# Performance work log

Hardware: AMD Instinct MI355X
Metric: run time of the kernel (lower is better)

The kernel has to match this reference:

```python
import jax, jax.numpy as jnp
import numpy as np

B, T, D_IN, D_PROJ, D_OUT, MEM = 8, 2048, 1024, 1024, 1024, 40


def setup_inputs() -> dict:
    key = jax.random.key(0)
    k1, k2, k3, k4 = jax.random.split(key, 4)
    x = jax.random.normal(k1, (B, T, D_IN), dtype=jnp.float32)
    # xavier-uniform-style params
    lim1 = np.sqrt(6.0 / (D_IN + D_PROJ))
    lim2 = np.sqrt(6.0 / (D_PROJ + D_OUT))
    limm = np.sqrt(6.0 / (MEM + 1 + D_PROJ))
    W1 = jax.random.uniform(k2, (D_IN, D_PROJ), minval=-lim1, maxval=lim1, dtype=jnp.float32)
    W2 = jax.random.uniform(k3, (D_PROJ, D_OUT), minval=-lim2, maxval=lim2, dtype=jnp.float32)
    mw = jax.random.uniform(k4, (MEM + 1, D_PROJ), minval=-limm, maxval=limm, dtype=jnp.float32)
    mw = mw.at[0].set(0.0)  # row 0 zeroed at init (still trainable in the original)
    bias1 = jnp.ones((D_PROJ,), dtype=jnp.float32)
    bias2 = jnp.ones((D_OUT,), dtype=jnp.float32)
    return {"input_data": x, "W1": W1, "bias1": bias1, "W2": W2, "bias2": bias2,
            "memory_weights": mw}


def _fsmn_memory(p, memory_weights):
    # p: [B, T, D], memory_weights: [M+1, D]
    # Original gather index: mm[i,j] = i-j+1 for 0<=i-j<=M-1, else 0.
    # => out[b,i,d] = sum_{l=0}^{M-1} w[l+1,d]*p[b,i-l,d]
    #              + w[0,d] * (sum_j p[b,j,d] - sum_{l=0}^{M-1} p[b,i-l,d])
    M = memory_weights.shape[0] - 1
    b, t, d = p.shape
    # causal depthwise conv: taps w[1:] with lag l -> kernel position M-1-l
    rhs = memory_weights[1:][::-1].T[:, None, :]           # [D, 1, M]
    lhs = jnp.pad(p.transpose(0, 2, 1), ((0, 0), (0, 0), (M - 1, 0)))  # [B, D, T+M-1]
    band = jax.lax.conv_general_dilated(
        lhs, rhs, window_strides=(1,), padding='VALID',
        feature_group_count=d,
        dimension_numbers=('NCH', 'OIH', 'NCH')).transpose(0, 2, 1)    # [B, T, D]
    # in-band running sum via cumsum difference
    cs = jnp.cumsum(p, axis=1)                              # [B, T, D]
    band_sum = cs - jnp.pad(cs, ((0, 0), (M, 0), (0, 0)))[:, :t]
    total = cs[:, -1:]                                      # [B, 1, D]
    return band + memory_weights[0] * (total - band_sum)


def reference(input_data, W1, bias1, W2, bias2, memory_weights):
    p = jnp.matmul(input_data, W1) + bias1                  # [B, T, D_PROJ]
    p = _fsmn_memory(p, memory_weights)
    return jnp.matmul(p, W2) + bias2                        # [B, T, D_OUT]
```

## Files before the change

kernel.cpp:

```cpp
#include <hip/hip_runtime.h>

typedef __attribute__((ext_vector_type(8))) short bf16x8;
typedef __attribute__((ext_vector_type(4))) float f32x4;
typedef __attribute__((ext_vector_type(8))) unsigned short u16x8;

typedef const __attribute__((address_space(1))) void* as1cv;
typedef __attribute__((address_space(3))) void* as3v;

__device__ __forceinline__ unsigned short f2bf(float f) {
    union { float f; unsigned u; } x; x.f = f;
    unsigned r = x.u + 0x7FFFu + ((x.u >> 16) & 1u);
    return (unsigned short)(r >> 16);
}
__device__ __forceinline__ float bf2f(unsigned short u) {
    union { unsigned u; float f; } x; x.u = ((unsigned)u) << 16; return x.f;
}

__global__ void k_cvt_bf16(const float* __restrict__ in, unsigned short* __restrict__ out, long n) {
    long i = (long)blockIdx.x * blockDim.x + threadIdx.x;
    long stride = (long)gridDim.x * blockDim.x;
    long n4 = n >> 2;
    for (long j = i; j < n4; j += stride) {
        float4 v = ((const float4*)in)[j];
        ushort4 o;
        o.x = f2bf(v.x); o.y = f2bf(v.y); o.z = f2bf(v.z); o.w = f2bf(v.w);
        ((ushort4*)out)[j] = o;
    }
}

__global__ void k_transpose_bf16(const float* __restrict__ W, unsigned short* __restrict__ Wt,
                                 int rows, int cols) {
    __shared__ float tile[64][65];
    int r0 = blockIdx.y * 64, c0 = blockIdx.x * 64;
    #pragma unroll
    for (int i = 0; i < 16; ++i) {
        int idx = threadIdx.x + i * 256;
        int r = idx >> 6, c = idx & 63;
        tile[r][c] = W[(long)(r0 + r) * cols + (c0 + c)];
    }
    __syncthreads();
    #pragma unroll
    for (int i = 0; i < 16; ++i) {
        int idx = threadIdx.x + i * 256;
        int r = idx >> 6, c = idx & 63;
        Wt[(long)(c0 + r) * rows + (r0 + c)] = f2bf(tile[c][r]);
    }
}

template<int OUT_BF16>
__global__ __launch_bounds__(512, 2) void k_gemm256(
    const unsigned short* __restrict__ A,
    const unsigned short* __restrict__ Bt,
    const float* __restrict__ bias,
    void* __restrict__ C,
    int M, int N, int K)
{
    __shared__ unsigned short lds[2][4][8192];
    const int tid  = threadIdx.x;
    const int lane = tid & 63;
    const int w    = tid >> 6;
    const int wm   = w >> 2;
    const int wn   = w & 3;

    const int nwg = gridDim.x;
    const int cpx = nwg >> 3;
    const int wg  = (blockIdx.x & 7) * cpx + (blockIdx.x >> 3);
    const int nblks = N >> 8;
    const int mblk = wg / nblks, nblk = wg % nblks;
    const long m0 = (long)mblk << 8, n0 = (long)nblk << 8;

    const int segRow  = lane >> 3;
    const long segColE = (long)(((lane & 7) ^ segRow) << 3);

    const int rr = lane & 15, cc = lane >> 4;
    const int smask = (rr & 7) << 4;
    const int colSwz0 = (((cc * 16) ^ smask) >> 1);
    const int colSwz1 = (((64 + cc * 16) ^ smask) >> 1);

    auto stage = [&](int buf, int slot, const unsigned short* src, long rowBase, int kt) {
        #pragma unroll
        for (int g = 0; g < 2; ++g) {
            const int s = w + g * 8;
            const unsigned short* gp = src + (rowBase + s * 8 + segRow) * (long)K
                                           + (long)kt * 64 + segColE;
            __builtin_amdgcn_global_load_lds((as1cv)gp,
                (as3v)(&lds[buf][slot][s * 512 + lane * 8]), 16, 0, 0);
        }
    };

    f32x4 acc[8][4];
    #pragma unroll
    for (int i = 0; i < 8; ++i)
        #pragma unroll
        for (int j = 0; j < 4; ++j)
            acc[i][j] = (f32x4){0.f, 0.f, 0.f, 0.f};

    bf16x8 bfrag[4][2];
    const int bRowBase = (wn & 1) * 64;
    const int NK = K >> 6;
    const int ITERS = K >> 7;

#define VM4   asm volatile("s_waitcnt vmcnt(4)" ::: "memory")
#define PHASE(BUF, Q, STAGES, VMW) do {                                              \
    bf16x8 af0_0, af0_1, af1_0, af1_1;                                               \
    { const unsigned short* Ah = &lds[BUF][wm][0];                                   \
      af0_0 = *(const bf16x8*)(Ah + ((Q)*32 + rr) * 64 + colSwz0);                   \
      af0_1 = *(const bf16x8*)(Ah + ((Q)*32 + rr) * 64 + colSwz1);                   \
      af1_0 = *(const bf16x8*)(Ah + ((Q)*32 + 16 + rr) * 64 + colSwz0);              \
      af1_1 = *(const bf16x8*)(Ah + ((Q)*32 + 16 + rr) * 64 + colSwz1); }            \
    if ((Q) == 0) { const unsigned short* Bh = &lds[BUF][2 + (wn >> 1)][0];          \
      _Pragma("unroll")                                                              \
      for (int nj = 0; nj < 4; ++nj) {                                               \
        bfrag[nj][0] = *(const bf16x8*)(Bh + (bRowBase + nj*16 + rr) * 64 + colSwz0);\
        bfrag[nj][1] = *(const bf16x8*)(Bh + (bRowBase + nj*16 + rr) * 64 + colSwz1);\
      } }                                                                            \
    STAGES;                                                                          \
    VMW;                                                                             \
    __builtin_amdgcn_s_barrier();                                                    \
    asm volatile("s_waitcnt lgkmcnt(0)" ::: "memory");                               \
    __builtin_amdgcn_sched_barrier(0);                                               \
    __builtin_amdgcn_s_setprio(1);                                                   \
    _Pragma("unroll")                                                                \
    for (int nj = 0; nj < 4; ++nj) {                                                 \
      acc[2*(Q)][nj]   = __builtin_amdgcn_mfma_f32_16x16x32_bf16(af0_0, bfrag[nj][0], acc[2*(Q)][nj],   0,0,0); \
      acc[2*(Q)][nj]   = __builtin_amdgcn_mfma_f32_16x16x32_bf16(af0_1, bfrag[nj][1], acc[2*(Q)][nj],   0,0,0); \
      acc[2*(Q)+1][nj] = __builtin_amdgcn_mfma_f32_16x16x32_bf16(af1_0, bfrag[nj][0], acc[2*(Q)+1][nj], 0,0,0); \
      acc[2*(Q)+1][nj] = __builtin_amdgcn_mfma_f32_16x16x32_bf16(af1_1, bfrag[nj][1], acc[2*(Q)+1][nj], 0,0,0); \
    }                                                                                \
    __builtin_amdgcn_s_setprio(0);                                                   \
    __builtin_amdgcn_s_barrier();                                                    \
} while (0)

    stage(0, 0, A,  m0,       0);
    stage(0, 1, A,  m0 + 128, 0);
    stage(0, 2, Bt, n0,       0);
    stage(0, 3, Bt, n0 + 128, 0);
    stage(1, 2, Bt, n0,       1);
    stage(1, 3, Bt, n0 + 128, 1);
    VM4;
    __builtin_amdgcn_s_barrier();

    for (int it = 0; it < ITERS; ++it) {
        const int kt1 = 2 * it + 1;
        int kt2 = 2 * it + 2; if (kt2 >= NK) kt2 = 0;
        int kt3 = 2 * it + 3; if (kt3 >= NK) kt3 = 1;

        PHASE(0, 0, stage(1, 0, A,  m0,       kt1), );
        PHASE(0, 1, stage(1, 1, A,  m0 + 128, kt1), );
        PHASE(0, 2, { stage(0, 2, Bt, n0, kt2); stage(0, 3, Bt, n0 + 128, kt2); }, );
        PHASE(0, 3, , VM4);
        PHASE(1, 0, stage(0, 0, A,  m0,       kt2), );
        PHASE(1, 1, stage(0, 1, A,  m0 + 128, kt2), );
        PHASE(1, 2, { stage(1, 2, Bt, n0, kt3); stage(1, 3, Bt, n0 + 128, kt3); }, );
        PHASE(1, 3, , VM4);
    }
#undef PHASE
#undef VM4

    #pragma unroll
    for (int mi = 0; mi < 8; ++mi) {
        const long rowb = m0 + wm * 128 + mi * 16 + cc * 4;
        #pragma unroll
        for (int nj = 0; nj < 4; ++nj) {
            const long col = n0 + wn * 64 + nj * 16 + rr;
            const float bv = bias[col];
            #pragma unroll
            for (int jj = 0; jj < 4; ++jj) {
                const float v = acc[mi][nj][jj] + bv;
                if (OUT_BF16) ((unsigned short*)C)[(rowb + jj) * N + col] = f2bf(v);
                else          ((float*)C)[(rowb + jj) * N + col] = v;
            }
        }
    }
}

__global__ void k_colsum(const unsigned short* __restrict__ p, float* __restrict__ total, int T) {
    const int b = blockIdx.y;
    const int t0 = blockIdx.x * 64;
    const int tid = threadIdx.x;
    float s0 = 0.f, s1 = 0.f, s2 = 0.f, s3 = 0.f;
    const unsigned short* base = p + ((long)b * T + t0) * 1024 + tid * 4;
    for (int t = 0; t < 64; ++t) {
        ushort4 v = *(const ushort4*)(base + (long)t * 1024);
        s0 += bf2f(v.x); s1 += bf2f(v.y); s2 += bf2f(v.z); s3 += bf2f(v.w);
    }
    float* tp = total + b * 1024 + tid * 4;
    atomicAdd(tp + 0, s0); atomicAdd(tp + 1, s1);
    atomicAdd(tp + 2, s2); atomicAdd(tp + 3, s3);
}

#define FS_ROWS 167
__global__ __launch_bounds__(256, 2) void k_fsmn(
    const unsigned short* __restrict__ p,
    const float* __restrict__ mw,
    const float* __restrict__ total,
    unsigned short* __restrict__ p2,
    int T)
{
    __shared__ unsigned short sp[FS_ROWS][64];
    __shared__ float smw[41][64];
    const int b  = blockIdx.z;
    const int t0 = blockIdx.y * 128;
    const int d0 = blockIdx.x * 64;
    const int tid = threadIdx.x;

    for (int idx = tid; idx < 41 * 64; idx += 256) {
        int r = idx >> 6, c = idx & 63;
        smw[r][c] = mw[r * 1024 + d0 + c];
    }
    {
        const int row0 = tid >> 3;
        const int col8 = (tid & 7) * 8;
        #pragma unroll
        for (int i = 0; i < 6; ++i) {
            const int row = row0 + i * 32;
            if (row < FS_ROWS) {
                const int t = t0 + row - 39;
                u16x8 v = {0, 0, 0, 0, 0, 0, 0, 0};
                if (t >= 0)
                    v = *(const u16x8*)(p + ((long)b * T + t) * 1024 + d0 + col8);
                *(u16x8*)(&sp[row][col8]) = v;
            }
        }
    }
    __syncthreads();

    const int lane = tid & 63, wv = tid >> 6;
    const int d = d0 + lane;

    float m[40];
    #pragma unroll
    for (int l = 0; l < 40; ++l) m[l] = smw[l + 1][lane];
    const float m0v = smw[0][lane];
    const float tot = total[b * 1024 + d];

    #pragma unroll
    for (int pass = 0; pass < 2; ++pass) {
        const int obase = wv * 32 + pass * 16;
        float w[55];
        #pragma unroll
        for (int j = 0; j < 55; ++j) w[j] = bf2f(sp[obase + j][lane]);

        float acc[16];
        #pragma unroll
        for (int s = 0; s < 16; ++s) acc[s] = 0.f;
        #pragma unroll
        for (int lag = 0; lag < 40; ++lag) {
            const float mm = m[lag];
            #pragma unroll
            for (int s = 0; s < 16; ++s)
                acc[s] = fmaf(mm, w[s + 39 - lag], acc[s]);
        }

        float accw[16];
        {
            float S = 0.f;
            #pragma unroll
            for (int j = 0; j < 40; ++j) S += w[j];
            accw[0] = S;
            #pragma unroll
            for (int s = 1; s < 16; ++s) accw[s] = accw[s - 1] + w[s + 39] - w[s - 1];
        }

        unsigned short* ob = p2 + ((long)b * T + t0 + obase) * 1024 + d;
        #pragma unroll
        for (int s = 0; s < 16; ++s)
            ob[(long)s * 1024] = f2bf(acc[s] + m0v * (tot - accw[s]));
    }
}

extern "C" void kernel_launch(void* const* d_in, const int* in_sizes, int n_in,
                              void* d_out, int out_size, void* d_ws, size_t ws_size,
                              hipStream_t stream) {
    const float* x  = (const float*)d_in[0];
    const float* W1 = (const float*)d_in[1];
    const float* b1 = (const float*)d_in[2];
    const float* W2 = (const float*)d_in[3];
    const float* b2 = (const float*)d_in[4];
    const float* mw = (const float*)d_in[5];
    float* out = (float*)d_out;

    const int B = 8, T = 2048;
    const long M = (long)B * T;
    const int N = 1024, K = 1024;

    char* ws = (char*)d_ws;
    unsigned short* x_bf   = (unsigned short*)(ws);
    unsigned short* W1t    = (unsigned short*)(ws + 33554432L);
    unsigned short* W2t    = (unsigned short*)(ws + 35651584L);
    unsigned short* p_bf   = (unsigned short*)(ws + 37748736L);
    float*          totals = (float*)(ws + 71303168L);
    unsigned short* p2_bf  = x_bf;

    k_cvt_bf16<<<2048, 256, 0, stream>>>(x, x_bf, M * 1024);

    dim3 tgrid(16, 16);
    k_transpose_bf16<<<tgrid, 256, 0, stream>>>(W1, W1t, K, N);
    k_transpose_bf16<<<tgrid, 256, 0, stream>>>(W2, W2t, K, N);

    k_gemm256<1><<<dim3((int)((M / 256) * (N / 256))), 512, 0, stream>>>(
        x_bf, W1t, b1, (void*)p_bf, (int)M, N, K);

    hipMemsetAsync(totals, 0, B * 1024 * sizeof(float), stream);
    k_colsum<<<dim3(T / 64, B), 256, 0, stream>>>(p_bf, totals, T);

    k_fsmn<<<dim3(1024 / 64, T / 128, B), 256, 0, stream>>>(p_bf, mw, totals, p2_bf, T);

    k_gemm256<0><<<dim3((int)((M / 256) * (N / 256))), 512, 0, stream>>>(
        p2_bf, W2t, b2, (void*)out, (int)M, N, K);
}
```

Measured before the change: 137.7 us.

## Fuse column-sum into first GEMM epilogue and vectorize stores via swapped MFMA operands

Swaps the MFMA operand order so each lane holds four consecutive output columns. The epilogue can then write packed bf16x4 or float4 stores instead of scalar ones. The first GEMM also reduces per-column sums across lanes and atomically adds them into the per-batch totals, so the separate colsum kernel and its re-read of p are removed. The two weight transposes are merged into one launch. Costs are more atomics from many blocks and a slightly heavier epilogue; the fused sums are taken in fp32 before bf16 rounding, which shifts numerics slightly.

```diff
diff --git a/kernel.cpp b/kernel.cpp
--- a/kernel.cpp
+++ b/kernel.cpp
@@ -28,8 +28,11 @@
     }
 }
 
-__global__ void k_transpose_bf16(const float* __restrict__ W, unsigned short* __restrict__ Wt,
-                                 int rows, int cols) {
+__global__ void k_transpose_bf16(const float* __restrict__ W1, unsigned short* __restrict__ W1t,
+                                 const float* __restrict__ W2, unsigned short* __restrict__ W2t) {
+    const int rows = 1024, cols = 1024;
+    const float* W = blockIdx.z ? W2 : W1;
+    unsigned short* Wt = blockIdx.z ? W2t : W1t;
     __shared__ float tile[64][65];
     int r0 = blockIdx.y * 64, c0 = blockIdx.x * 64;
     #pragma unroll
@@ -47,12 +50,13 @@
     }
 }
 
-template<int OUT_BF16>
+template<int OUT_BF16, int DO_COLSUM>
 __global__ __launch_bounds__(512, 2) void k_gemm256(
     const unsigned short* __restrict__ A,
     const unsigned short* __restrict__ Bt,
     const float* __restrict__ bias,
     void* __restrict__ C,
+    float* __restrict__ totals,
     int M, int N, int K)
 {
     __shared__ unsigned short lds[2][4][8192];
@@ -88,11 +92,11 @@
         }
     };
 
-    f32x4 acc[8][4];
-    #pragma unroll
-    for (int i = 0; i < 8; ++i)
-        #pragma unroll
-        for (int j = 0; j < 4; ++j)
+    f32x4 acc[4][8];
+    #pragma unroll
+    for (int i = 0; i < 4; ++i)
+        #pragma unroll
+        for (int j = 0; j < 8; ++j)
             acc[i][j] = (f32x4){0.f, 0.f, 0.f, 0.f};
 
     bf16x8 bfrag[4][2];
@@ -122,10 +126,10 @@
     __builtin_amdgcn_s_setprio(1);                                                   \
     _Pragma("unroll")                                                                \
     for (int nj = 0; nj < 4; ++nj) {                                                 \
-      acc[2*(Q)][nj]   = __builtin_amdgcn_mfma_f32_16x16x32_bf16(af0_0, bfrag[nj][0], acc[2*(Q)][nj],   0,0,0); \
-      acc[2*(Q)][nj]   = __builtin_amdgcn_mfma_f32_16x16x32_bf16(af0_1, bfrag[nj][1], acc[2*(Q)][nj],   0,0,0); \
-      acc[2*(Q)+1][nj] = __builtin_amdgcn_mfma_f32_16x16x32_bf16(af1_0, bfrag[nj][0], acc[2*(Q)+1][nj], 0,0,0); \
-      acc[2*(Q)+1][nj] = __builtin_amdgcn_mfma_f32_16x16x32_bf16(af1_1, bfrag[nj][1], acc[2*(Q)+1][nj], 0,0,0); \
+      acc[nj][2*(Q)]   = __builtin_amdgcn_mfma_f32_16x16x32_bf16(bfrag[nj][0], af0_0, acc[nj][2*(Q)],   0,0,0); \
+      acc[nj][2*(Q)]   = __builtin_amdgcn_mfma_f32_16x16x32_bf16(bfrag[nj][1], af0_1, acc[nj][2*(Q)],   0,0,0); \
+      acc[nj][2*(Q)+1] = __builtin_amdgcn_mfma_f32_16x16x32_bf16(bfrag[nj][0], af1_0, acc[nj][2*(Q)+1], 0,0,0); \
+      acc[nj][2*(Q)+1] = __builtin_amdgcn_mfma_f32_16x16x32_bf16(bfrag[nj][1], af1_1, acc[nj][2*(Q)+1], 0,0,0); \
     }                                                                                \
     __builtin_amdgcn_s_setprio(0);                                                   \
     __builtin_amdgcn_s_barrier();                                                    \
@@ -158,35 +162,43 @@
 #undef VM4
 
     #pragma unroll
-    for (int mi = 0; mi < 8; ++mi) {
-        const long rowb = m0 + wm * 128 + mi * 16 + cc * 4;
-        #pragma unroll
-        for (int nj = 0; nj < 4; ++nj) {
-            const long col = n0 + wn * 64 + nj * 16 + rr;
-            const float bv = bias[col];
+    for (int nj = 0; nj < 4; ++nj) {
+        const long colb = n0 + wn * 64 + nj * 16 + cc * 4;
+        const float4 bv4 = *(const float4*)(bias + colb);
+        float cs0 = 0.f, cs1 = 0.f, cs2 = 0.f, cs3 = 0.f;
+        #pragma unroll
+        for (int ri = 0; ri < 8; ++ri) {
+            const long row = m0 + wm * 128 + ri * 16 + rr;
+            const f32x4 v = acc[nj][ri];
+            const float o0 = v[0] + bv4.x, o1 = v[1] + bv4.y;
+            const float o2 = v[2] + bv4.z, o3 = v[3] + bv4.w;
+            if (DO_COLSUM) { cs0 += o0; cs1 += o1; cs2 += o2; cs3 += o3; }
+            if (OUT_BF16) {
+                uint2 pk;
+                pk.x = ((unsigned)f2bf(o1) << 16) | f2bf(o0);
+                pk.y = ((unsigned)f2bf(o3) << 16) | f2bf(o2);
+                *(uint2*)((unsigned short*)C + row * N + colb) = pk;
+            } else {
+                float4 pk = {o0, o1, o2, o3};
+                *(float4*)((float*)C + row * N + colb) = pk;
+            }
+        }
+        if (DO_COLSUM) {
             #pragma unroll
-            for (int jj = 0; jj < 4; ++jj) {
-                const float v = acc[mi][nj][jj] + bv;
-                if (OUT_BF16) ((unsigned short*)C)[(rowb + jj) * N + col] = f2bf(v);
-                else          ((float*)C)[(rowb + jj) * N + col] = v;
+            for (int s = 1; s < 16; s <<= 1) {
+                cs0 += __shfl_xor(cs0, s, 64);
+                cs1 += __shfl_xor(cs1, s, 64);
+                cs2 += __shfl_xor(cs2, s, 64);
+                cs3 += __shfl_xor(cs3, s, 64);
             }
-        }
-    }
-}
-
-__global__ void k_colsum(const unsigned short* __restrict__ p, float* __restrict__ total, int T) {
-    const int b = blockIdx.y;
-    const int t0 = blockIdx.x * 64;
-    const int tid = threadIdx.x;
-    float s0 = 0.f, s1 = 0.f, s2 = 0.f, s3 = 0.f;
-    const unsigned short* base = p + ((long)b * T + t0) * 1024 + tid * 4;
-    for (int t = 0; t < 64; ++t) {
-        ushort4 v = *(const ushort4*)(base + (long)t * 1024);
-        s0 += bf2f(v.x); s1 += bf2f(v.y); s2 += bf2f(v.z); s3 += bf2f(v.w);
-    }
-    float* tp = total + b * 1024 + tid * 4;
-    atomicAdd(tp + 0, s0); atomicAdd(tp + 1, s1);
-    atomicAdd(tp + 2, s2); atomicAdd(tp + 3, s3);
+            if (rr == 0) {
+                const int b = (int)(m0 >> 11);
+                float* tp = totals + b * 1024 + colb;
+                atomicAdd(tp + 0, cs0); atomicAdd(tp + 1, cs1);
+                atomicAdd(tp + 2, cs2); atomicAdd(tp + 3, cs3);
+            }
+        }
+    }
 }
 
 #define FS_ROWS 167
@@ -294,18 +306,15 @@
 
     k_cvt_bf16<<<2048, 256, 0, stream>>>(x, x_bf, M * 1024);
 
-    dim3 tgrid(16, 16);
-    k_transpose_bf16<<<tgrid, 256, 0, stream>>>(W1, W1t, K, N);
-    k_transpose_bf16<<<tgrid, 256, 0, stream>>>(W2, W2t, K, N);
-
-    k_gemm256<1><<<dim3((int)((M / 256) * (N / 256))), 512, 0, stream>>>(
-        x_bf, W1t, b1, (void*)p_bf, (int)M, N, K);
+    k_transpose_bf16<<<dim3(16, 16, 2), 256, 0, stream>>>(W1, W1t, W2, W2t);
 
     hipMemsetAsync(totals, 0, B * 1024 * sizeof(float), stream);
-    k_colsum<<<dim3(T / 64, B), 256, 0, stream>>>(p_bf, totals, T);
+
+    k_gemm256<1, 1><<<dim3((int)((M / 256) * (N / 256))), 512, 0, stream>>>(
+        x_bf, W1t, b1, (void*)p_bf, totals, (int)M, N, K);
 
     k_fsmn<<<dim3(1024 / 64, T / 128, B), 256, 0, stream>>>(p_bf, mw, totals, p2_bf, T);
 
-    k_gemm256<0><<<dim3((int)((M / 256) * (N / 256))), 512, 0, stream>>>(
-        p2_bf, W2t, b2, (void*)out, (int)M, N, K);
-}
+    k_gemm256<0, 0><<<dim3((int)((M / 256) * (N / 256))), 512, 0, stream>>>(
+        p2_bf, W2t, b2, (void*)out, nullptr, (int)M, N, K);
+}
```

Result: no change. 136.7 us (-0.7%).

## Fuse column-sum into first GEMM epilogue and merge weight transposes

Applied to the files above, without the earlier changes.

Removes the separate colsum kernel by accumulating per-column sums inside the first GEMM epilogue, using cross-lane shuffles and one atomicAdd per column per tile. The two weight transposes become one launch indexed by blockIdx.z. The MFMA issue order is also changed to interleave the k-halves. The column sums now use fp32 values before bf16 rounding, which changes numerics slightly, and the epilogue loop order is swapped.

```diff
diff --git a/kernel.cpp b/kernel.cpp
--- a/kernel.cpp
+++ b/kernel.cpp
@@ -28,8 +28,11 @@
     }
 }
 
-__global__ void k_transpose_bf16(const float* __restrict__ W, unsigned short* __restrict__ Wt,
-                                 int rows, int cols) {
+__global__ void k_transpose_bf16(const float* __restrict__ W1, unsigned short* __restrict__ W1t,
+                                 const float* __restrict__ W2, unsigned short* __restrict__ W2t) {
+    const int rows = 1024, cols = 1024;
+    const float* W = blockIdx.z ? W2 : W1;
+    unsigned short* Wt = blockIdx.z ? W2t : W1t;
     __shared__ float tile[64][65];
     int r0 = blockIdx.y * 64, c0 = blockIdx.x * 64;
     #pragma unroll
@@ -47,12 +50,13 @@
     }
 }
 
-template<int OUT_BF16>
+template<int OUT_BF16, int DO_COLSUM>
 __global__ __launch_bounds__(512, 2) void k_gemm256(
     const unsigned short* __restrict__ A,
     const unsigned short* __restrict__ Bt,
     const float* __restrict__ bias,
     void* __restrict__ C,
+    float* __restrict__ totals,
     int M, int N, int K)
 {
     __shared__ unsigned short lds[2][4][8192];
@@ -102,12 +106,12 @@
 
 #define VM4   asm volatile("s_waitcnt vmcnt(4)" ::: "memory")
 #define PHASE(BUF, Q, STAGES, VMW) do {                                              \
-    bf16x8 af0_0, af0_1, af1_0, af1_1;                                               \
+    bf16x8 af0[2], af1[2];                                                           \
     { const unsigned short* Ah = &lds[BUF][wm][0];                                   \
-      af0_0 = *(const bf16x8*)(Ah + ((Q)*32 + rr) * 64 + colSwz0);                   \
-      af0_1 = *(const bf16x8*)(Ah + ((Q)*32 + rr) * 64 + colSwz1);                   \
-      af1_0 = *(const bf16x8*)(Ah + ((Q)*32 + 16 + rr) * 64 + colSwz0);              \
-      af1_1 = *(const bf16x8*)(Ah + ((Q)*32 + 16 + rr) * 64 + colSwz1); }            \
+      af0[0] = *(const bf16x8*)(Ah + ((Q)*32 + rr) * 64 + colSwz0);                  \
+      af0[1] = *(const bf16x8*)(Ah + ((Q)*32 + rr) * 64 + colSwz1);                  \
+      af1[0] = *(const bf16x8*)(Ah + ((Q)*32 + 16 + rr) * 64 + colSwz0);             \
+      af1[1] = *(const bf16x8*)(Ah + ((Q)*32 + 16 + rr) * 64 + colSwz1); }           \
     if ((Q) == 0) { const unsigned short* Bh = &lds[BUF][2 + (wn >> 1)][0];          \
       _Pragma("unroll")                                                              \
       for (int nj = 0; nj < 4; ++nj) {                                               \
@@ -121,12 +125,12 @@
     __builtin_amdgcn_sched_barrier(0);                                               \
     __builtin_amdgcn_s_setprio(1);                                                   \
     _Pragma("unroll")                                                                \
-    for (int nj = 0; nj < 4; ++nj) {                                                 \
-      acc[2*(Q)][nj]   = __builtin_amdgcn_mfma_f32_16x16x32_bf16(af0_0, bfrag[nj][0], acc[2*(Q)][nj],   0,0,0); \
-      acc[2*(Q)][nj]   = __builtin_amdgcn_mfma_f32_16x16x32_bf16(af0_1, bfrag[nj][1], acc[2*(Q)][nj],   0,0,0); \
-      acc[2*(Q)+1][nj] = __builtin_amdgcn_mfma_f32_16x16x32_bf16(af1_0, bfrag[nj][0], acc[2*(Q)+1][nj], 0,0,0); \
-      acc[2*(Q)+1][nj] = __builtin_amdgcn_mfma_f32_16x16x32_bf16(af1_1, bfrag[nj][1], acc[2*(Q)+1][nj], 0,0,0); \
-    }                                                                                \
+    for (int k = 0; k < 2; ++k)                                                      \
+      _Pragma("unroll")                                                              \
+      for (int nj = 0; nj < 4; ++nj) {                                               \
+        acc[2*(Q)][nj]   = __builtin_amdgcn_mfma_f32_16x16x32_bf16(af0[k], bfrag[nj][k], acc[2*(Q)][nj],   0,0,0); \
+        acc[2*(Q)+1][nj] = __builtin_amdgcn_mfma_f32_16x16x32_bf16(af1[k], bfrag[nj][k], acc[2*(Q)+1][nj], 0,0,0); \
+      }                                                                              \
     __builtin_amdgcn_s_setprio(0);                                                   \
     __builtin_amdgcn_s_barrier();                                                    \
 } while (0)
@@ -157,36 +161,32 @@
 #undef PHASE
 #undef VM4
 
-    #pragma unroll
-    for (int mi = 0; mi < 8; ++mi) {
-        const long rowb = m0 + wm * 128 + mi * 16 + cc * 4;
-        #pragma unroll
-        for (int nj = 0; nj < 4; ++nj) {
-            const long col = n0 + wn * 64 + nj * 16 + rr;
-            const float bv = bias[col];
+    const long rowb0 = m0 + wm * 128 + cc * 4;
+    #pragma unroll
+    for (int nj = 0; nj < 4; ++nj) {
+        const long col = n0 + wn * 64 + nj * 16 + rr;
+        const float bv = bias[col];
+        float cs = 0.f;
+        #pragma unroll
+        for (int mi = 0; mi < 8; ++mi) {
+            const long rowb = rowb0 + mi * 16;
             #pragma unroll
             for (int jj = 0; jj < 4; ++jj) {
                 const float v = acc[mi][nj][jj] + bv;
+                if (DO_COLSUM) cs += v;
                 if (OUT_BF16) ((unsigned short*)C)[(rowb + jj) * N + col] = f2bf(v);
                 else          ((float*)C)[(rowb + jj) * N + col] = v;
             }
         }
-    }
-}
-
-__global__ void k_colsum(const unsigned short* __restrict__ p, float* __restrict__ total, int T) {
-    const int b = blockIdx.y;
-    const int t0 = blockIdx.x * 64;
-    const int tid = threadIdx.x;
-    float s0 = 0.f, s1 = 0.f, s2 = 0.f, s3 = 0.f;
-    const unsigned short* base = p + ((long)b * T + t0) * 1024 + tid * 4;
-    for (int t = 0; t < 64; ++t) {
-        ushort4 v = *(const ushort4*)(base + (long)t * 1024);
-        s0 += bf2f(v.x); s1 += bf2f(v.y); s2 += bf2f(v.z); s3 += bf2f(v.w);
-    }
-    float* tp = total + b * 1024 + tid * 4;
-    atomicAdd(tp + 0, s0); atomicAdd(tp + 1, s1);
-    atomicAdd(tp + 2, s2); atomicAdd(tp + 3, s3);
+        if (DO_COLSUM) {
+            cs += __shfl_xor(cs, 16, 64);
+            cs += __shfl_xor(cs, 32, 64);
+            if (cc == 0) {
+                const int b = (int)(m0 >> 11);
+                atomicAdd(totals + b * 1024 + col, cs);
+            }
+        }
+    }
 }
 
 #define FS_ROWS 167
@@ -294,18 +294,15 @@
 
     k_cvt_bf16<<<2048, 256, 0, stream>>>(x, x_bf, M * 1024);
 
-    dim3 tgrid(16, 16);
-    k_transpose_bf16<<<tgrid, 256, 0, stream>>>(W1, W1t, K, N);
-    k_transpose_bf16<<<tgrid, 256, 0, stream>>>(W2, W2t, K, N);
-
-    k_gemm256<1><<<dim3((int)((M / 256) * (N / 256))), 512, 0, stream>>>(
-        x_bf, W1t, b1, (void*)p_bf, (int)M, N, K);
+    k_transpose_bf16<<<dim3(16, 16, 2), 256, 0, stream>>>(W1, W1t, W2, W2t);
 
     hipMemsetAsync(totals, 0, B * 1024 * sizeof(float), stream);
-    k_colsum<<<dim3(T / 64, B), 256, 0, stream>>>(p_bf, totals, T);
+
+    k_gemm256<1, 1><<<dim3((int)((M / 256) * (N / 256))), 512, 0, stream>>>(
+        x_bf, W1t, b1, (void*)p_bf, totals, (int)M, N, K);
 
     k_fsmn<<<dim3(1024 / 64, T / 128, B), 256, 0, stream>>>(p_bf, mw, totals, p2_bf, T);
 
-    k_gemm256<0><<<dim3((int)((M / 256) * (N / 256))), 512, 0, stream>>>(
-        p2_bf, W2t, b2, (void*)out, (int)M, N, K);
-}
+    k_gemm256<0, 0><<<dim3((int)((M / 256) * (N / 256))), 512, 0, stream>>>(
+        p2_bf, W2t, b2, (void*)out, nullptr, (int)M, N, K);
+}
```

New measurement: 136.2 us. Within noise of the previous version (-1.1%).
